# Performance work log

Measured on AMD Instinct MI355X. Metric: run time of the kernel, lower is better.

The kernel has to match this reference:

```python
import jax, jax.numpy as jnp
import numpy as np
import math

EPS = 1e-5

def _layernorm(x, g, b):
    m = x.mean(-1, keepdims=True)
    v = ((x - m) ** 2).mean(-1, keepdims=True)
    return (x - m) / jnp.sqrt(v + EPS) * g + b

def _skew(emd):
    # RelativePositionalEmbed pad/cat/view skew trick. emd: (B,H,S,S)
    B, H, S, _ = emd.shape
    x = jnp.concatenate([emd, jnp.zeros_like(emd)], -1)   # (B,H,S,2S)
    x = x.reshape(B, H, -1)                                # (B,H,2*S*S)
    l = 2 * S - 1
    extra = (-x.shape[-1]) % l
    x = jnp.concatenate([x, jnp.zeros((B, H, extra), x.dtype)], -1)
    x = x.reshape(B, H, -1, l)
    return x[..., :S, S - 1:]                              # (B,H,S,S)

def setup_inputs() -> dict:
    key = jax.random.key(0)
    ks = jax.random.split(key, 8)
    S, B, D, H, DFF = 1024, 4, 1024, 16, 4096
    dh = D // H
    sc = 1.0 / math.sqrt(D)
    return {
        'x': jax.random.normal(ks[0], (S, B, D), jnp.float32),
        'wq': jax.random.normal(ks[1], (D, D), jnp.float32) * sc,
        'wk': jax.random.normal(ks[2], (D, D), jnp.float32) * sc,
        'wv': jax.random.normal(ks[3], (D, D), jnp.float32) * sc,
        'rel_w': jax.random.normal(ks[4], (B, H, dh, S), jnp.float32) * (1.0 / math.sqrt(dh)),
        'ln1_g': jnp.ones((D,), jnp.float32),
        'ln1_b': jnp.zeros((D,), jnp.float32),
        'ln2_g': jnp.ones((D,), jnp.float32),
        'ln2_b': jnp.zeros((D,), jnp.float32),
        'w1_w': jax.random.normal(ks[5], (DFF, D), jnp.float32) * sc,
        'w1_b': jnp.zeros((DFF,), jnp.float32),
        'w2_w': jax.random.normal(ks[6], (D, DFF), jnp.float32) * (1.0 / math.sqrt(DFF)),
        'w2_b': jnp.zeros((D,), jnp.float32),
    }

def reference(x, wq, wk, wv, rel_w, ln1_g, ln1_b, ln2_g, ln2_b, w1_w, w1_b, w2_w, w2_b):
    S, B, D = x.shape
    H = rel_w.shape[1]
    dh = D // H

    def proj(w):
        y = x @ w.T                      # (S,B,D)
        # torch .view(B,S,H,dh): raw row-major reinterpretation, not a transpose
        return y.reshape(B, S, H, dh).swapaxes(1, 2)  # (B,H,S,dh)

    q, k, v = proj(wq), proj(wk), proj(wv)
    scores = jnp.einsum('bhsd,bhtd->bhst', q * (1.0 / math.sqrt(dh)), k)  # (B,H,S,S)
    # mask=False path: the on-the-fly linear1/linear2 reprojection of qk is
    # computed then discarded in the original; omitted here (dead code).
    emd = jnp.einsum('bhsd,bhdt->bhst', q, rel_w)
    scores = scores + _skew(emd)
    attn = jax.nn.softmax(scores, axis=0)            # softmax over BATCH dim, as in source
    out = jnp.einsum('bhst,bhtd->bhsd', attn, v)     # (B,H,S,dh)
    attn_out = out.reshape(S, B, D)                  # raw reshape, as in source
    h1 = _layernorm(x + attn_out, ln1_g, ln1_b)      # dropout = identity (eval)
    ffn = jnp.maximum(h1 @ w1_w.T + w1_b, 0.0) @ w2_w.T + w2_b
    return _layernorm(h1 + ffn, ln2_g, ln2_b)
```

## Files before the change

### kernel.cpp

```cpp
#include <hip/hip_runtime.h>


typedef unsigned short u16;
typedef unsigned int u32;
typedef __attribute__((ext_vector_type(4))) float f32x4;
typedef __attribute__((ext_vector_type(8))) short bf16x8;
typedef __attribute__((ext_vector_type(4))) u32 u32x4;

__device__ __forceinline__ float bf2f(u16 u) { return __uint_as_float(((u32)u) << 16); }
__device__ __forceinline__ u16 f2bf(float f) {
    u32 u = __float_as_uint(f);
    u += 0x7fffu + ((u >> 16) & 1u);
    return (u16)(u >> 16);
}
__device__ __forceinline__ u32 cvtpk(float lo, float hi) {
    u32 r;
    asm("v_cvt_pk_bf16_f32 %0, %1, %2" : "=v"(r) : "v"(lo), "v"(hi));
    return r;
}
template<int DT>
__device__ __forceinline__ float load1(const void* P, size_t idx) {
    return (DT == 0) ? bf2f(((const u16*)P)[idx]) : ((const float*)P)[idx];
}

__global__ __launch_bounds__(256) void sentinel_ws(float* out, u32 n)
{
    for (u32 i = blockIdx.x * 256 + threadIdx.x; i < n; i += gridDim.x * 256) out[i] = 31000.0f;
}

__global__ __launch_bounds__(256) void cvt_f32_bf16(const float* __restrict__ s,
                                                    u16* __restrict__ d, u32 n)
{
    u32 i = (blockIdx.x * 256 + threadIdx.x) * 4;
    if (i >= n) return;
    float4 v = *(const float4*)(s + i);
    uint2 pk;
    pk.x = (u32)f2bf(v.x) | ((u32)f2bf(v.y) << 16);
    pk.y = (u32)f2bf(v.z) | ((u32)f2bf(v.w) << 16);
    *(uint2*)(d + i) = pk;
}

__global__ __launch_bounds__(256) void relw_tr(const float* __restrict__ relw,
                                               u16* __restrict__ relwT)
{
    __shared__ __align__(16) float T[64][68];
    const int tid = threadIdx.x;
    const int bh = blockIdx.y;
    const int u0 = blockIdx.x << 6;
    {
        const int d = tid >> 2, uq = (tid & 3) << 4;
        const float* rp = relw + (size_t)bh * 65536 + (size_t)d * 1024 + u0 + uq;
#pragma unroll
        for (int i = 0; i < 4; i++)
            *(float4*)&T[d][uq + i * 4] = *(const float4*)(rp + i * 4);
    }
    __syncthreads();
    {
        const int u = tid >> 2, dq = (tid & 3) << 4;
        u32 pk[8];
#pragma unroll
        for (int p = 0; p < 8; p++)
            pk[p] = cvtpk(T[dq + p * 2][u], T[dq + p * 2 + 1][u]);
        u16* op = relwT + ((size_t)(bh * 1024 + u0 + u) << 6) + dq;
        *(uint4*)op = *(uint4*)&pk[0];
        *(uint4*)(op + 8) = *(uint4*)&pk[4];
    }
}

__global__ __launch_bounds__(256) void yv_tr(const u16* __restrict__ Yv,
                                             u16* __restrict__ YvT)
{
    __shared__ __align__(16) u16 T[64][72];
    const int tid = threadIdx.x;
    const int bh = blockIdx.y, b = bh >> 4, h = bh & 15;
    const int t0 = blockIdx.x << 6;
    {
        const int r = tid >> 2, cq = (tid & 3) << 4;
        const u16* p = Yv + ((size_t)(b * 1024 + t0 + r) << 10) + h * 64 + cq;
        *(uint4*)&T[r][cq] = *(const uint4*)p;
        *(uint4*)&T[r][cq + 8] = *(const uint4*)(p + 8);
    }
    __syncthreads();
    {
        const int d = tid >> 2, tq = (tid & 3) << 4;
        u16 vals[16];
#pragma unroll
        for (int p = 0; p < 16; p++) vals[p] = T[tq + p][d];
        u16* op = YvT + (((size_t)bh * 64 + d) << 10) + t0 + tq;
        *(uint4*)op = ((uint4*)vals)[0];
        *(uint4*)(op + 8) = ((uint4*)vals)[1];
    }
}

template<int RELU, int OUT_F32, int HAS_BIAS>
__global__ __launch_bounds__(256) void mfma_gemm(
    const u16* __restrict__ A, const u16* __restrict__ B,
    const float* __restrict__ bias, void* __restrict__ Cout,
    int M, int N, int K)
{
    __shared__ __align__(16) u16 As[4096];
    __shared__ __align__(16) u16 Bs[4096];
    const int tid = threadIdx.x;
    const int wave = tid >> 6, lane = tid & 63;
    const int quad = lane >> 4, l16 = lane & 15;
    const int m0 = blockIdx.y << 7, n0 = blockIdx.x << 7;
    const int wm = (wave >> 1) << 6, wn = (wave & 1) << 6;

    const int r0 = tid >> 2;
    const int csw = ((tid & 3) ^ ((r0 >> 1) & 3)) << 3;
    const u16* Ag0 = A + (size_t)(m0 + r0) * K + csw;
    const u16* Ag1 = A + (size_t)(m0 + r0 + 64) * K + csw;
    const u16* Bg0 = B + (size_t)(n0 + r0) * K + csw;
    const u16* Bg1 = B + (size_t)(n0 + r0 + 64) * K + csw;

    f32x4 acc[4][4];
#pragma unroll
    for (int i = 0; i < 4; i++)
#pragma unroll
        for (int j = 0; j < 4; j++) acc[i][j] = (f32x4){0.f, 0.f, 0.f, 0.f};

    const int pb = ((quad ^ ((l16 >> 1) & 3)) << 3);

    uint4 a0 = *(const uint4*)(Ag0);
    uint4 a1 = *(const uint4*)(Ag1);
    uint4 b0 = *(const uint4*)(Bg0);
    uint4 b1 = *(const uint4*)(Bg1);

    for (int k0 = 0; k0 < K; k0 += 32) {
        __syncthreads();
        *(uint4*)(As + tid * 8)        = a0;
        *(uint4*)(As + 2048 + tid * 8) = a1;
        *(uint4*)(Bs + tid * 8)        = b0;
        *(uint4*)(Bs + 2048 + tid * 8) = b1;
        __syncthreads();

        if (k0 + 32 < K) {
            a0 = *(const uint4*)(Ag0 + k0 + 32);
            a1 = *(const uint4*)(Ag1 + k0 + 32);
            b0 = *(const uint4*)(Bg0 + k0 + 32);
            b1 = *(const uint4*)(Bg1 + k0 + 32);
        }

        bf16x8 af[4], bfr[4];
#pragma unroll
        for (int mi = 0; mi < 4; mi++)
            af[mi] = *(const bf16x8*)(As + ((wm + mi * 16 + l16) << 5) + pb);
#pragma unroll
        for (int ni = 0; ni < 4; ni++)
            bfr[ni] = *(const bf16x8*)(Bs + ((wn + ni * 16 + l16) << 5) + pb);
#pragma unroll
        for (int mi = 0; mi < 4; mi++)
#pragma unroll
            for (int ni = 0; ni < 4; ni++)
                acc[mi][ni] = __builtin_amdgcn_mfma_f32_16x16x32_bf16(
                    af[mi], bfr[ni], acc[mi][ni], 0, 0, 0);
    }

    float bb[4];
#pragma unroll
    for (int ni = 0; ni < 4; ni++)
        bb[ni] = HAS_BIAS ? bias[n0 + wn + ni * 16 + l16] : 0.f;

#pragma unroll
    for (int mi = 0; mi < 4; mi++) {
#pragma unroll
        for (int ni = 0; ni < 4; ni++) {
            const int col = n0 + wn + ni * 16 + l16;
#pragma unroll
            for (int r = 0; r < 4; r++) {
                const int row = m0 + wm + mi * 16 + quad * 4 + r;
                float v = acc[mi][ni][r] + bb[ni];
                if (RELU) v = fmaxf(v, 0.f);
                if (OUT_F32) ((float*)Cout)[(size_t)row * N + col] = v;
                else ((u16*)Cout)[(size_t)row * N + col] = f2bf(v);
            }
        }
    }
}

__global__ __launch_bounds__(256) void qk_strip(
    const u16* __restrict__ Yq, const u16* __restrict__ Yk,
    const u16* __restrict__ relwT, u16* __restrict__ scores)
{
    __shared__ __align__(16) u16 lds[27008];
    u16* Ks  = lds;
    u16* Rw  = lds + 4608;
    u16* Eb  = lds + 13824;
    u16* Ssh = lds + 22400;

    const int tid = threadIdx.x;
    const int wave = tid >> 6, lane = tid & 63;
    const int quad = lane >> 4, l16 = lane & 15;
    const int ws = wave >> 1, wt = wave & 1;

    const int linb = blockIdx.y * 16 + blockIdx.x;
    const int swz = (linb & 7) * 128 + (linb >> 3);
    const int si = swz & 15, bh = swz >> 4;
    const int b = bh >> 4, h = bh & 15;
    const int s0 = si << 6;
    const int qb0 = 15 - si;
    const int tau0 = 2 + wt * 2 - ws * 2;

    bf16x8 qf[2][2];
#pragma unroll
    for (int mi = 0; mi < 2; mi++)
#pragma unroll
        for (int kk = 0; kk < 2; kk++)
            qf[mi][kk] = *(const bf16x8*)(Yq +
                ((size_t)(b * 1024 + s0 + ws * 32 + mi * 16 + l16) << 10) +
                h * 64 + kk * 32 + quad * 8);

    const int r = tid >> 2, cq = (tid & 3) << 4;
    const u16* Kg = Yk + ((size_t)(b * 1024 + r) << 10) + h * 64 + cq;
    const u16* Rg = relwT + ((size_t)bh << 16) + cq;

    uint4 kp0, kp1, rp0, rp1, ri0, ri1;
    kp0 = *(const uint4*)(Kg);
    kp1 = *(const uint4*)(Kg + 8);
    {
        const u16* p = Rg + ((size_t)(960 - s0 + r) << 6);
        ri0 = *(const uint4*)p; ri1 = *(const uint4*)(p + 8);
    }
    {
        const int u = 1024 - s0 + r;
        uint4 z = {0, 0, 0, 0};
        rp0 = z; rp1 = z;
        if (u < 1024) {
            const u16* p = Rg + ((size_t)u << 6);
            rp0 = *(const uint4*)p; rp1 = *(const uint4*)(p + 8);
        }
    }

    for (int i = 0; i < 16; i++) {
        const int t0 = i << 6;
        __syncthreads();
        *(uint4*)(Ks + r * 72 + cq)     = kp0;
        *(uint4*)(Ks + r * 72 + cq + 8) = kp1;
        if (i == 0) {
            u16* hb = Rw + (qb0 & 1) * 4608;
            *(uint4*)(hb + r * 72 + cq)     = ri0;
            *(uint4*)(hb + r * 72 + cq + 8) = ri1;
        }
        if (i <= si) {
            u16* hb = Rw + ((qb0 + i + 1) & 1) * 4608;
            *(uint4*)(hb + r * 72 + cq)     = rp0;
            *(uint4*)(hb + r * 72 + cq + 8) = rp1;
        }
        __syncthreads();

        if (i + 1 < 16) {
            const u16* p = Kg + ((size_t)(i + 1) << 16);
            kp0 = *(const uint4*)p; kp1 = *(const uint4*)(p + 8);
        }
        if (i + 1 <= si) {
            const int u = 1024 - s0 + ((i + 1) << 6) + r;
            uint4 z = {0, 0, 0, 0};
            rp0 = z; rp1 = z;
            if (u < 1024) {
                const u16* p = Rg + ((size_t)u << 6);
                rp0 = *(const uint4*)p; rp1 = *(const uint4*)(p + 8);
            }
        }

        f32x4 aqk[2][2];
#pragma unroll
        for (int mi = 0; mi < 2; mi++)
#pragma unroll
            for (int nj = 0; nj < 2; nj++) aqk[mi][nj] = (f32x4){0.f, 0.f, 0.f, 0.f};
#pragma unroll
        for (int kk = 0; kk < 2; kk++)
#pragma unroll
            for (int nj = 0; nj < 2; nj++) {
                bf16x8 kb = *(const bf16x8*)(Ks + (wt * 32 + nj * 16 + l16) * 72 +
                                             kk * 32 + quad * 8);
#pragma unroll
                for (int mi = 0; mi < 2; mi++)
                    aqk[mi][nj] = __builtin_amdgcn_mfma_f32_16x16x32_bf16(
                        qf[mi][kk], kb, aqk[mi][nj], 0, 0, 0);
            }

        const int eact = (i <= si);
        if (eact) {
            const int qb = qb0 + i;
            f32x4 ae[4][2];
#pragma unroll
            for (int uj = 0; uj < 4; uj++)
#pragma unroll
                for (int mi = 0; mi < 2; mi++) ae[uj][mi] = (f32x4){0.f, 0.f, 0.f, 0.f};
#pragma unroll
            for (int kk = 0; kk < 2; kk++)
#pragma unroll
                for (int uj = 0; uj < 4; uj++) {
                    const int tau = tau0 + uj;
                    const u16* hp = Rw + ((qb + (tau >> 2)) & 1) * 4608;
                    bf16x8 ra = *(const bf16x8*)(hp + ((tau & 3) * 16 + l16) * 72 +
                                                 kk * 32 + quad * 8);
#pragma unroll
                    for (int mi = 0; mi < 2; mi++)
                        ae[uj][mi] = __builtin_amdgcn_mfma_f32_16x16x32_bf16(
                            ra, qf[mi][kk], ae[uj][mi], 0, 0, 0);
                }
#pragma unroll
            for (int uj = 0; uj < 4; uj++)
#pragma unroll
                for (int mi = 0; mi < 2; mi++) {
                    const int scol = ws * 32 + mi * 16 + l16;
                    const int cb = (tau0 + uj) * 16 + quad * 4;
                    uint2 pk;
                    pk.x = cvtpk(ae[uj][mi][0], ae[uj][mi][1]);
                    pk.y = cvtpk(ae[uj][mi][2], ae[uj][mi][3]);
                    *(uint2*)(Eb + scol * 134 + cb) = pk;
                }
        }

#pragma unroll
        for (int mi = 0; mi < 2; mi++)
#pragma unroll
            for (int nj = 0; nj < 2; nj++) {
                const int slb = ws * 32 + mi * 16 + quad * 4;
                const int tl = wt * 32 + nj * 16 + l16;
                float v[4];
#pragma unroll
                for (int rr = 0; rr < 4; rr++) {
                    const int sl = slb + rr;
                    float e = 0.f;
                    if (eact) e = bf2f(Eb[sl * 133 + 63 + tl]);
                    v[rr] = aqk[mi][nj][rr] * 0.125f + e;
                }
                const u32 r01 = cvtpk(v[0], v[1]);
                const u32 r23 = cvtpk(v[2], v[3]);
                Ssh[(slb + 0) * 72 + tl] = (u16)r01;
                Ssh[(slb + 1) * 72 + tl] = (u16)(r01 >> 16);
                Ssh[(slb + 2) * 72 + tl] = (u16)r23;
                Ssh[(slb + 3) * 72 + tl] = (u16)(r23 >> 16);
            }

        {
            const int row = ws * 32 + (lane >> 1);
            const int col = wt * 32 + ((lane & 1) << 4);
            uint4 v0 = *(const uint4*)(Ssh + row * 72 + col);
            uint4 v1 = *(const uint4*)(Ssh + row * 72 + col + 8);
            u16* op = scores + (((size_t)bh * 1024 + s0 + row) << 10) + t0 + col;
            *(uint4*)op = v0;
            *(uint4*)(op + 8) = v1;
        }
    }
}

__global__ __launch_bounds__(256) void pv_smx(
    const u16* __restrict__ scraw, const u16* __restrict__ YvT,
    float* __restrict__ O)
{
    __shared__ __align__(16) u16 Vt[18432];
    const int tid = threadIdx.x;
    const int w = tid >> 6, lane = tid & 63;
    const int quad = lane >> 4, l16 = lane & 15;

    const int bid = blockIdx.x;
    const int swz = (bid & 7) * 32 + (bid >> 3);
    const int h = swz >> 4, si = swz & 15;
    const int s0 = si << 6;

    const u16* Pl = scraw + ((size_t)(h * 1024 + s0 + w * 16 + l16) << 10) + quad * 8;
    const int sr0 = tid >> 3, sc0 = (tid & 7) << 3;
    const u16* Vg = YvT + ((size_t)h << 16) + ((size_t)sr0 << 10) + sc0;

    f32x4 acc[4][4];
#pragma unroll
    for (int b = 0; b < 4; b++)
#pragma unroll
        for (int j = 0; j < 4; j++) acc[b][j] = (f32x4){0.f, 0.f, 0.f, 0.f};

    u32x4 pc[4][2], pn[4][2], vc[4][2], vn[4][2];
#pragma unroll
    for (int b = 0; b < 4; b++) {
        pc[b][0] = *(const u32x4*)(Pl + ((size_t)b << 24));
        pc[b][1] = *(const u32x4*)(Pl + ((size_t)b << 24) + 32);
        vc[b][0] = *(const u32x4*)(Vg + ((size_t)b << 20));
        vc[b][1] = *(const u32x4*)(Vg + ((size_t)b << 20) + (32 << 10));
    }

    for (int t0 = 0; t0 < 1024; t0 += 64) {
        __syncthreads();
#pragma unroll
        for (int b = 0; b < 4; b++) {
            *(u32x4*)(Vt + b * 4608 + sr0 * 72 + sc0)        = vc[b][0];
            *(u32x4*)(Vt + b * 4608 + (sr0 + 32) * 72 + sc0) = vc[b][1];
        }
        __syncthreads();

        const int more = (t0 + 64 < 1024);
        if (more) {
#pragma unroll
            for (int b = 0; b < 4; b++) {
                pn[b][0] = *(const u32x4*)(Pl + ((size_t)b << 24) + t0 + 64);
                pn[b][1] = *(const u32x4*)(Pl + ((size_t)b << 24) + t0 + 96);
                vn[b][0] = *(const u32x4*)(Vg + ((size_t)b << 20) + t0 + 64);
                vn[b][1] = *(const u32x4*)(Vg + ((size_t)b << 20) + (32 << 10) + t0 + 64);
            }
        }

#pragma unroll
        for (int kk = 0; kk < 2; kk++) {
            u32x4 aw[4];
#pragma unroll
            for (int j = 0; j < 4; j++) {
                float x0[4], x1[4];
#pragma unroll
                for (int b = 0; b < 4; b++) {
                    const u32 wd = pc[b][kk][j];
                    x0[b] = __uint_as_float(wd << 16);
                    x1[b] = __uint_as_float(wd & 0xffff0000u);
                }
                const float m0 = fmaxf(fmaxf(x0[0], x0[1]), fmaxf(x0[2], x0[3]));
                const float m1 = fmaxf(fmaxf(x1[0], x1[1]), fmaxf(x1[2], x1[3]));
                float s0v = 0.f, s1v = 0.f;
#pragma unroll
                for (int b = 0; b < 4; b++) {
                    x0[b] = __expf(x0[b] - m0); s0v += x0[b];
                    x1[b] = __expf(x1[b] - m1); s1v += x1[b];
                }
                const float r0 = 1.f / s0v, r1 = 1.f / s1v;
#pragma unroll
                for (int b = 0; b < 4; b++)
                    aw[b][j] = cvtpk(x0[b] * r0, x1[b] * r1);
            }
#pragma unroll
            for (int b = 0; b < 4; b++) {
                const bf16x8 af = __builtin_bit_cast(bf16x8, aw[b]);
#pragma unroll
                for (int nj = 0; nj < 4; nj++) {
                    bf16x8 bv = *(const bf16x8*)(Vt + b * 4608 + (nj * 16 + l16) * 72 +
                                                 kk * 32 + quad * 8);
                    acc[b][nj] = __builtin_amdgcn_mfma_f32_16x16x32_bf16(
                        af, bv, acc[b][nj], 0, 0, 0);
                }
            }
        }

        if (more) {
#pragma unroll
            for (int b = 0; b < 4; b++) {
                pc[b][0] = pn[b][0]; pc[b][1] = pn[b][1];
                vc[b][0] = vn[b][0]; vc[b][1] = vn[b][1];
            }
        }
    }

#pragma unroll
    for (int b = 0; b < 4; b++)
#pragma unroll
        for (int nj = 0; nj < 4; nj++)
#pragma unroll
            for (int rr = 0; rr < 4; rr++) {
                const int row = s0 + w * 16 + quad * 4 + rr;
                O[((((size_t)(b * 16 + h) << 10) + row) << 6) + nj * 16 + l16] =
                    acc[b][nj][rr];
            }
}

template<int DTA, int OUT_F32>
__global__ __launch_bounds__(256) void add_ln(
    const void* __restrict__ A, const float* __restrict__ Bf,
    const float* __restrict__ g, const float* __restrict__ beta,
    void* __restrict__ out)
{
    const int row = blockIdx.x;
    const int tid = threadIdx.x;
    const size_t base = (size_t)row * 1024;
    float v[4], s1 = 0.f, s2 = 0.f;
#pragma unroll
    for (int k = 0; k < 4; k++) {
        const int c = k * 256 + tid;
        float t = load1<DTA>(A, base + c) + Bf[base + c];
        v[k] = t; s1 += t; s2 += t * t;
    }
#pragma unroll
    for (int m = 1; m < 64; m <<= 1) {
        s1 += __shfl_xor(s1, m, 64);
        s2 += __shfl_xor(s2, m, 64);
    }
    __shared__ float red[8];
    if ((tid & 63) == 0) { red[(tid >> 6) * 2] = s1; red[(tid >> 6) * 2 + 1] = s2; }
    __syncthreads();
    s1 = red[0] + red[2] + red[4] + red[6];
    s2 = red[1] + red[3] + red[5] + red[7];
    const float mean = s1 * (1.f / 1024.f);
    const float var = s2 * (1.f / 1024.f) - mean * mean;
    const float rstd = rsqrtf(var + 1e-5f);
#pragma unroll
    for (int k = 0; k < 4; k++) {
        const int c = k * 256 + tid;
        float o = (v[k] - mean) * rstd * g[c] + beta[c];
        if (OUT_F32) ((float*)out)[base + c] = o;
        else ((u16*)out)[base + c] = f2bf(o);
    }
}

extern "C" void kernel_launch(void* const* d_in, const int* in_sizes, int n_in,
                              void* d_out, int out_size, void* d_ws, size_t ws_size,
                              hipStream_t stream)
{
    const float* x    = (const float*)d_in[0];
    const float* wq   = (const float*)d_in[1];
    const float* wk   = (const float*)d_in[2];
    const float* wv   = (const float*)d_in[3];
    const float* relw = (const float*)d_in[4];
    const float* g1   = (const float*)d_in[5];
    const float* be1  = (const float*)d_in[6];
    const float* g2   = (const float*)d_in[7];
    const float* be2  = (const float*)d_in[8];
    const float* w1   = (const float*)d_in[9];
    const float* b1   = (const float*)d_in[10];
    const float* w2   = (const float*)d_in[11];
    const float* b2   = (const float*)d_in[12];

    const size_t NEEDED = ((size_t)224 << 20);
    if (ws_size < NEEDED) {
        sentinel_ws<<<dim3(1024), dim3(256), 0, stream>>>((float*)d_out, (u32)out_size);
        return;
    }

    char* ws = (char*)d_ws;
    float* O     = (float*)(ws);
    u16*   relwT = (u16*)(ws);
    u16*   Yq    = (u16*)(ws + ((size_t)16 << 20));
    u16*   Yk    = (u16*)(ws + ((size_t)24 << 20));
    u16*   Yv    = (u16*)(ws + ((size_t)32 << 20));
    u16*   h1    = (u16*)(ws + ((size_t)40 << 20));
    u16*   ffn1  = (u16*)(ws + ((size_t)48 << 20));
    float* ffn2  = (float*)(ws + ((size_t)80 << 20));
    u16*   YvT   = (u16*)(ws + ((size_t)80 << 20));
    u16*   sc    = (u16*)(ws + ((size_t)96 << 20));
    u16*   xb    = (u16*)(ws + ((size_t)96 << 20));
    u16*   wqb   = (u16*)(ws + ((size_t)104 << 20));
    u16*   wkb   = (u16*)(ws + ((size_t)106 << 20));
    u16*   wvb   = (u16*)(ws + ((size_t)108 << 20));
    u16*   w1b   = (u16*)(ws + ((size_t)96 << 20));
    u16*   w2b   = (u16*)(ws + ((size_t)104 << 20));

    dim3 blk(256);
    const u32 M4 = 4u << 20, M1 = 1u << 20;

    cvt_f32_bf16<<<dim3(M4 / 1024), blk, 0, stream>>>(x,  xb,  M4);
    cvt_f32_bf16<<<dim3(M1 / 1024), blk, 0, stream>>>(wq, wqb, M1);
    cvt_f32_bf16<<<dim3(M1 / 1024), blk, 0, stream>>>(wk, wkb, M1);
    cvt_f32_bf16<<<dim3(M1 / 1024), blk, 0, stream>>>(wv, wvb, M1);
    relw_tr<<<dim3(16, 64), blk, 0, stream>>>(relw, relwT);

    mfma_gemm<0,0,0><<<dim3(8, 32), blk, 0, stream>>>(xb, wqb, nullptr, Yq, 4096, 1024, 1024);
    mfma_gemm<0,0,0><<<dim3(8, 32), blk, 0, stream>>>(xb, wkb, nullptr, Yk, 4096, 1024, 1024);
    mfma_gemm<0,0,0><<<dim3(8, 32), blk, 0, stream>>>(xb, wvb, nullptr, Yv, 4096, 1024, 1024);
    yv_tr<<<dim3(16, 64), blk, 0, stream>>>(Yv, YvT);

    qk_strip<<<dim3(16, 64), blk, 0, stream>>>(Yq, Yk, relwT, sc);
    pv_smx<<<dim3(256), blk, 0, stream>>>(sc, YvT, O);

    add_ln<1,0><<<dim3(4096), blk, 0, stream>>>(x, O, g1, be1, h1);

    cvt_f32_bf16<<<dim3(M4 / 1024), blk, 0, stream>>>(w1, w1b, M4);
    cvt_f32_bf16<<<dim3(M4 / 1024), blk, 0, stream>>>(w2, w2b, M4);

    mfma_gemm<1,0,1><<<dim3(32, 32), blk, 0, stream>>>(h1, w1b, b1, ffn1, 4096, 4096, 1024);
    mfma_gemm<0,1,1><<<dim3(8, 32), blk, 0, stream>>>(ffn1, w2b, b2, ffn2, 4096, 1024, 4096);

    add_ln<0,1><<<dim3(4096), blk, 0, stream>>>(h1, ffn2, g2, be2, (float*)d_out);
}
```

Baseline: 485.3 us.

## Double-buffer GEMM tiles via direct global-to-LDS loads, drop cvt_pk asm

The GEMM kernel now uses two LDS buffers and global_load_lds so the next K-tile streams straight into shared memory while the current tile is consumed. This removes the register staging round-trip and one of the two barriers per iteration. It also replaces the inline v_cvt_pk_bf16_f32 asm with software round-to-nearest-even packing in several kernels. The software packing costs more ALU instructions, and LDS use in the GEMM doubles, which may lower occupancy.

```diff
diff --git a/kernel.cpp b/kernel.cpp
--- a/kernel.cpp
+++ b/kernel.cpp
@@ -13,15 +13,15 @@
     u += 0x7fffu + ((u >> 16) & 1u);
     return (u16)(u >> 16);
 }
-__device__ __forceinline__ u32 cvtpk(float lo, float hi) {
-    u32 r;
-    asm("v_cvt_pk_bf16_f32 %0, %1, %2" : "=v"(r) : "v"(lo), "v"(hi));
-    return r;
-}
 template<int DT>
 __device__ __forceinline__ float load1(const void* P, size_t idx) {
     return (DT == 0) ? bf2f(((const u16*)P)[idx]) : ((const float*)P)[idx];
 }
+
+#define GL16(gp, lp)                                                        \
+    __builtin_amdgcn_global_load_lds(                                       \
+        (const __attribute__((address_space(1))) void*)(gp),                \
+        (__attribute__((address_space(3))) void*)(lp), 16, 0, 0)
 
 __global__ __launch_bounds__(256) void sentinel_ws(float* out, u32 n)
 {
@@ -59,8 +59,10 @@
         const int u = tid >> 2, dq = (tid & 3) << 4;
         u32 pk[8];
 #pragma unroll
-        for (int p = 0; p < 8; p++)
-            pk[p] = cvtpk(T[dq + p * 2][u], T[dq + p * 2 + 1][u]);
+        for (int p = 0; p < 8; p++) {
+            float a = T[dq + p * 2][u], b = T[dq + p * 2 + 1][u];
+            pk[p] = (u32)f2bf(a) | ((u32)f2bf(b) << 16);
+        }
         u16* op = relwT + ((size_t)(bh * 1024 + u0 + u) << 6) + dq;
         *(uint4*)op = *(uint4*)&pk[0];
         *(uint4*)(op + 8) = *(uint4*)&pk[4];
@@ -98,8 +100,8 @@
     const float* __restrict__ bias, void* __restrict__ Cout,
     int M, int N, int K)
 {
-    __shared__ __align__(16) u16 As[4096];
-    __shared__ __align__(16) u16 Bs[4096];
+    __shared__ __align__(16) u16 As[2][4096];
+    __shared__ __align__(16) u16 Bs[2][4096];
     const int tid = threadIdx.x;
     const int wave = tid >> 6, lane = tid & 63;
     const int quad = lane >> 4, l16 = lane & 15;
@@ -121,39 +123,38 @@
 
     const int pb = ((quad ^ ((l16 >> 1) & 3)) << 3);
 
-    uint4 a0 = *(const uint4*)(Ag0);
-    uint4 a1 = *(const uint4*)(Ag1);
-    uint4 b0 = *(const uint4*)(Bg0);
-    uint4 b1 = *(const uint4*)(Bg1);
-
+    GL16(Ag0, &As[0][tid * 8]);
+    GL16(Ag1, &As[0][2048 + tid * 8]);
+    GL16(Bg0, &Bs[0][tid * 8]);
+    GL16(Bg1, &Bs[0][2048 + tid * 8]);
+    __syncthreads();
+
+    int cur = 0;
     for (int k0 = 0; k0 < K; k0 += 32) {
-        __syncthreads();
-        *(uint4*)(As + tid * 8)        = a0;
-        *(uint4*)(As + 2048 + tid * 8) = a1;
-        *(uint4*)(Bs + tid * 8)        = b0;
-        *(uint4*)(Bs + 2048 + tid * 8) = b1;
-        __syncthreads();
-
         if (k0 + 32 < K) {
-            a0 = *(const uint4*)(Ag0 + k0 + 32);
-            a1 = *(const uint4*)(Ag1 + k0 + 32);
-            b0 = *(const uint4*)(Bg0 + k0 + 32);
-            b1 = *(const uint4*)(Bg1 + k0 + 32);
+            const int nb = cur ^ 1;
+            GL16(Ag0 + k0 + 32, &As[nb][tid * 8]);
+            GL16(Ag1 + k0 + 32, &As[nb][2048 + tid * 8]);
+            GL16(Bg0 + k0 + 32, &Bs[nb][tid * 8]);
+            GL16(Bg1 + k0 + 32, &Bs[nb][2048 + tid * 8]);
         }
 
         bf16x8 af[4], bfr[4];
 #pragma unroll
         for (int mi = 0; mi < 4; mi++)
-            af[mi] = *(const bf16x8*)(As + ((wm + mi * 16 + l16) << 5) + pb);
+            af[mi] = *(const bf16x8*)(&As[cur][((wm + mi * 16 + l16) << 5) + pb]);
 #pragma unroll
         for (int ni = 0; ni < 4; ni++)
-            bfr[ni] = *(const bf16x8*)(Bs + ((wn + ni * 16 + l16) << 5) + pb);
+            bfr[ni] = *(const bf16x8*)(&Bs[cur][((wn + ni * 16 + l16) << 5) + pb]);
 #pragma unroll
         for (int mi = 0; mi < 4; mi++)
 #pragma unroll
             for (int ni = 0; ni < 4; ni++)
                 acc[mi][ni] = __builtin_amdgcn_mfma_f32_16x16x32_bf16(
                     af[mi], bfr[ni], acc[mi][ni], 0, 0, 0);
+
+        __syncthreads();
+        cur ^= 1;
     }
 
     float bb[4];
@@ -307,8 +308,8 @@
                     const int scol = ws * 32 + mi * 16 + l16;
                     const int cb = (tau0 + uj) * 16 + quad * 4;
                     uint2 pk;
-                    pk.x = cvtpk(ae[uj][mi][0], ae[uj][mi][1]);
-                    pk.y = cvtpk(ae[uj][mi][2], ae[uj][mi][3]);
+                    pk.x = (u32)f2bf(ae[uj][mi][0]) | ((u32)f2bf(ae[uj][mi][1]) << 16);
+                    pk.y = (u32)f2bf(ae[uj][mi][2]) | ((u32)f2bf(ae[uj][mi][3]) << 16);
                     *(uint2*)(Eb + scol * 134 + cb) = pk;
                 }
         }
@@ -316,24 +317,15 @@
 #pragma unroll
         for (int mi = 0; mi < 2; mi++)
 #pragma unroll
-            for (int nj = 0; nj < 2; nj++) {
-                const int slb = ws * 32 + mi * 16 + quad * 4;
-                const int tl = wt * 32 + nj * 16 + l16;
-                float v[4];
+            for (int nj = 0; nj < 2; nj++)
 #pragma unroll
                 for (int rr = 0; rr < 4; rr++) {
-                    const int sl = slb + rr;
+                    const int sl = ws * 32 + mi * 16 + quad * 4 + rr;
+                    const int tl = wt * 32 + nj * 16 + l16;
                     float e = 0.f;
                     if (eact) e = bf2f(Eb[sl * 133 + 63 + tl]);
-                    v[rr] = aqk[mi][nj][rr] * 0.125f + e;
+                    Ssh[sl * 72 + tl] = f2bf(aqk[mi][nj][rr] * 0.125f + e);
                 }
-                const u32 r01 = cvtpk(v[0], v[1]);
-                const u32 r23 = cvtpk(v[2], v[3]);
-                Ssh[(slb + 0) * 72 + tl] = (u16)r01;
-                Ssh[(slb + 1) * 72 + tl] = (u16)(r01 >> 16);
-                Ssh[(slb + 2) * 72 + tl] = (u16)r23;
-                Ssh[(slb + 3) * 72 + tl] = (u16)(r23 >> 16);
-            }
 
         {
             const int row = ws * 32 + (lane >> 1);
@@ -423,7 +415,7 @@
                 const float r0 = 1.f / s0v, r1 = 1.f / s1v;
 #pragma unroll
                 for (int b = 0; b < 4; b++)
-                    aw[b][j] = cvtpk(x0[b] * r0, x1[b] * r1);
+                    aw[b][j] = (u32)f2bf(x0[b] * r0) | ((u32)f2bf(x1[b] * r1) << 16);
             }
 #pragma unroll
             for (int b = 0; b < 4; b++) {
```

Result: slower. 519.0 us (+6.9%).

## Fuse Q/K/V projections into one GEMM launch and drop packed bf16 convert asm

Applied to the files above, without the earlier changes.

Replaces the three separate Q, K and V projection GEMMs with a single launch over N=3072. It relies on the bf16 copies of wq, wk and wv sitting contiguously in the workspace. A SPLIT3 epilogue sends each 1024-column slice to its own output buffer, 4M elements apart. This cuts launch count and gives a larger grid for better CU fill. It also swaps the inline v_cvt_pk_bf16_f32 asm for software round-to-nearest packing, which costs more ALU work. Separately, the LDS strides of the relative-embedding staging buffer are shrunk, which changes its bank-access pattern.

```diff
diff --git a/kernel.cpp b/kernel.cpp
--- a/kernel.cpp
+++ b/kernel.cpp
@@ -12,11 +12,6 @@
     u32 u = __float_as_uint(f);
     u += 0x7fffu + ((u >> 16) & 1u);
     return (u16)(u >> 16);
-}
-__device__ __forceinline__ u32 cvtpk(float lo, float hi) {
-    u32 r;
-    asm("v_cvt_pk_bf16_f32 %0, %1, %2" : "=v"(r) : "v"(lo), "v"(hi));
-    return r;
 }
 template<int DT>
 __device__ __forceinline__ float load1(const void* P, size_t idx) {
@@ -59,8 +54,10 @@
         const int u = tid >> 2, dq = (tid & 3) << 4;
         u32 pk[8];
 #pragma unroll
-        for (int p = 0; p < 8; p++)
-            pk[p] = cvtpk(T[dq + p * 2][u], T[dq + p * 2 + 1][u]);
+        for (int p = 0; p < 8; p++) {
+            float a = T[dq + p * 2][u], b = T[dq + p * 2 + 1][u];
+            pk[p] = (u32)f2bf(a) | ((u32)f2bf(b) << 16);
+        }
         u16* op = relwT + ((size_t)(bh * 1024 + u0 + u) << 6) + dq;
         *(uint4*)op = *(uint4*)&pk[0];
         *(uint4*)(op + 8) = *(uint4*)&pk[4];
@@ -92,7 +89,7 @@
     }
 }
 
-template<int RELU, int OUT_F32, int HAS_BIAS>
+template<int RELU, int OUT_F32, int HAS_BIAS, int SPLIT3>
 __global__ __launch_bounds__(256) void mfma_gemm(
     const u16* __restrict__ A, const u16* __restrict__ B,
     const float* __restrict__ bias, void* __restrict__ Cout,
@@ -166,13 +163,18 @@
 #pragma unroll
         for (int ni = 0; ni < 4; ni++) {
             const int col = n0 + wn + ni * 16 + l16;
+            const size_t cb = SPLIT3
+                ? (((size_t)(col >> 10) << 22) + (size_t)(col & 1023))
+                : (size_t)col;
 #pragma unroll
             for (int r = 0; r < 4; r++) {
                 const int row = m0 + wm + mi * 16 + quad * 4 + r;
                 float v = acc[mi][ni][r] + bb[ni];
                 if (RELU) v = fmaxf(v, 0.f);
-                if (OUT_F32) ((float*)Cout)[(size_t)row * N + col] = v;
-                else ((u16*)Cout)[(size_t)row * N + col] = f2bf(v);
+                const size_t idx = SPLIT3 ? (cb + ((size_t)row << 10))
+                                          : ((size_t)row * N + cb);
+                if (OUT_F32) ((float*)Cout)[idx] = v;
+                else ((u16*)Cout)[idx] = f2bf(v);
             }
         }
     }
@@ -182,11 +184,11 @@
     const u16* __restrict__ Yq, const u16* __restrict__ Yk,
     const u16* __restrict__ relwT, u16* __restrict__ scores)
 {
-    __shared__ __align__(16) u16 lds[27008];
+    __shared__ __align__(16) u16 lds[26880];
     u16* Ks  = lds;
     u16* Rw  = lds + 4608;
     u16* Eb  = lds + 13824;
-    u16* Ssh = lds + 22400;
+    u16* Ssh = lds + 22272;
 
     const int tid = threadIdx.x;
     const int wave = tid >> 6, lane = tid & 63;
@@ -307,33 +309,24 @@
                     const int scol = ws * 32 + mi * 16 + l16;
                     const int cb = (tau0 + uj) * 16 + quad * 4;
                     uint2 pk;
-                    pk.x = cvtpk(ae[uj][mi][0], ae[uj][mi][1]);
-                    pk.y = cvtpk(ae[uj][mi][2], ae[uj][mi][3]);
-                    *(uint2*)(Eb + scol * 134 + cb) = pk;
+                    pk.x = (u32)f2bf(ae[uj][mi][0]) | ((u32)f2bf(ae[uj][mi][1]) << 16);
+                    pk.y = (u32)f2bf(ae[uj][mi][2]) | ((u32)f2bf(ae[uj][mi][3]) << 16);
+                    *(uint2*)(Eb + scol * 132 + cb) = pk;
                 }
         }
 
 #pragma unroll
         for (int mi = 0; mi < 2; mi++)
 #pragma unroll
-            for (int nj = 0; nj < 2; nj++) {
-                const int slb = ws * 32 + mi * 16 + quad * 4;
-                const int tl = wt * 32 + nj * 16 + l16;
-                float v[4];
+            for (int nj = 0; nj < 2; nj++)
 #pragma unroll
                 for (int rr = 0; rr < 4; rr++) {
-                    const int sl = slb + rr;
+                    const int sl = ws * 32 + mi * 16 + quad * 4 + rr;
+                    const int tl = wt * 32 + nj * 16 + l16;
                     float e = 0.f;
-                    if (eact) e = bf2f(Eb[sl * 133 + 63 + tl]);
-                    v[rr] = aqk[mi][nj][rr] * 0.125f + e;
+                    if (eact) e = bf2f(Eb[sl * 131 + 63 + tl]);
+                    Ssh[sl * 72 + tl] = f2bf(aqk[mi][nj][rr] * 0.125f + e);
                 }
-                const u32 r01 = cvtpk(v[0], v[1]);
-                const u32 r23 = cvtpk(v[2], v[3]);
-                Ssh[(slb + 0) * 72 + tl] = (u16)r01;
-                Ssh[(slb + 1) * 72 + tl] = (u16)(r01 >> 16);
-                Ssh[(slb + 2) * 72 + tl] = (u16)r23;
-                Ssh[(slb + 3) * 72 + tl] = (u16)(r23 >> 16);
-            }
 
         {
             const int row = ws * 32 + (lane >> 1);
@@ -423,7 +416,7 @@
                 const float r0 = 1.f / s0v, r1 = 1.f / s1v;
 #pragma unroll
                 for (int b = 0; b < 4; b++)
-                    aw[b][j] = cvtpk(x0[b] * r0, x1[b] * r1);
+                    aw[b][j] = (u32)f2bf(x0[b] * r0) | ((u32)f2bf(x1[b] * r1) << 16);
             }
 #pragma unroll
             for (int b = 0; b < 4; b++) {
@@ -548,9 +541,8 @@
     cvt_f32_bf16<<<dim3(M1 / 1024), blk, 0, stream>>>(wv, wvb, M1);
     relw_tr<<<dim3(16, 64), blk, 0, stream>>>(relw, relwT);
 
-    mfma_gemm<0,0,0><<<dim3(8, 32), blk, 0, stream>>>(xb, wqb, nullptr, Yq, 4096, 1024, 1024);
-    mfma_gemm<0,0,0><<<dim3(8, 32), blk, 0, stream>>>(xb, wkb, nullptr, Yk, 4096, 1024, 1024);
-    mfma_gemm<0,0,0><<<dim3(8, 32), blk, 0, stream>>>(xb, wvb, nullptr, Yv, 4096, 1024, 1024);
+    mfma_gemm<0,0,0,1><<<dim3(24, 32), blk, 0, stream>>>(
+        xb, wqb, nullptr, Yq, 4096, 3072, 1024);
     yv_tr<<<dim3(16, 64), blk, 0, stream>>>(Yv, YvT);
 
     qk_strip<<<dim3(16, 64), blk, 0, stream>>>(Yq, Yk, relwT, sc);
@@ -561,8 +553,8 @@
     cvt_f32_bf16<<<dim3(M4 / 1024), blk, 0, stream>>>(w1, w1b, M4);
     cvt_f32_bf16<<<dim3(M4 / 1024), blk, 0, stream>>>(w2, w2b, M4);
 
-    mfma_gemm<1,0,1><<<dim3(32, 32), blk, 0, stream>>>(h1, w1b, b1, ffn1, 4096, 4096, 1024);
-    mfma_gemm<0,1,1><<<dim3(8, 32), blk, 0, stream>>>(ffn1, w2b, b2, ffn2, 4096, 1024, 4096);
+    mfma_gemm<1,0,1,0><<<dim3(32, 32), blk, 0, stream>>>(h1, w1b, b1, ffn1, 4096, 4096, 1024);
+    mfma_gemm<0,1,1,0><<<dim3(8, 32), blk, 0, stream>>>(ffn1, w2b, b2, ffn2, 4096, 1024, 4096);
 
     add_ln<0,1><<<dim3(4096), blk, 0, stream>>>(h1, ffn2, g2, be2, (float*)d_out);
 }
```

Result: faster. 433.1 us (-10.8%).
